# Kernel tuning notes

Hardware: AMD Instinct MI355X
Metric: run time of the kernel (lower is better)

The kernel has to match this reference:

```python
import jax, jax.numpy as jnp
import numpy as np

KSIZE = 3
STRIDE = 1
NEG_INF = -jnp.inf


def semiconv_maxmin(x, kernel, stride=STRIDE):
    """Tropical (max-min) 2D convolution, 'same' padding with -inf.

    out[n,o,i,j] = max over (c,kh,kw) of min(x_pad[n,c,i*s+kh,j*s+kw], kernel[o,c,kh,kw])
    """
    N, C, H, W = x.shape
    O, _, K, _ = kernel.shape
    p = K - 1
    top = p // 2
    bottom = p - top
    xp = jnp.pad(x, ((0, 0), (0, 0), (top, bottom), (top, bottom)),
                 constant_values=NEG_INF)
    Ho = (H + p - K) // stride + 1
    Wo = (W + p - K) // stride + 1
    out = jnp.full((N, O, Ho, Wo), NEG_INF, dtype=x.dtype)
    # Unrolled loop over the K*K taps (small, fixed); vectorized over n,o,c,h,w.
    for kh in range(K):
        for kw in range(K):
            xs = xp[:, :, kh:kh + stride * Ho:stride, kw:kw + stride * Wo:stride]  # [N,C,Ho,Wo]
            w = kernel[:, :, kh, kw]                                # [O,C]
            cand = jnp.minimum(xs[:, None], w[None, :, :, None, None])  # [N,O,C,Ho,Wo]
            out = jnp.maximum(out, jnp.max(cand, axis=2))
    return out


def setup_inputs() -> dict:
    key = jax.random.key(0)
    k1, k2 = jax.random.split(key)
    x = jax.random.normal(k1, (8, 32, 112, 112), dtype=jnp.float32)
    kernel = jax.random.normal(k2, (32, 32, KSIZE, KSIZE), dtype=jnp.float32)
    return {"x": x, "kernel": kernel}


def reference(x, kernel):
    return semiconv_maxmin(x, kernel, STRIDE)
```

## Files before the change

### kernel.cpp

```cpp
#include <hip/hip_runtime.h>
#include <math.h>

#define C_IN  32
#define O_OUT 32
#define HIMG  112
#define WIMG  112
#define HW    (HIMG * WIMG)
#define TS    8
#define NCP   16
#define XROW  12
#define XPLANE (10 * XROW)
#define WSLOT 12
#define WSTRIDE 196
#define OBLK  16
#define NW    (O_OUT * NCP * WSLOT)

typedef _Float16 h2 __attribute__((ext_vector_type(2)));

static __device__ __forceinline__ h2 h2min(h2 a, h2 b) {
    h2 r; asm("v_pk_min_f16 %0, %1, %2" : "=v"(r) : "v"(a), "v"(b)); return r;
}
static __device__ __forceinline__ h2 h2max(h2 a, h2 b) {
    h2 r; asm("v_pk_max_f16 %0, %1, %2" : "=v"(r) : "v"(a), "v"(b)); return r;
}

static __device__ __forceinline__ h2 asH2(float f) {
    union { float f; h2 h; } u; u.f = f; return u.h;
}
static __device__ __forceinline__ float asF(h2 h) {
    union { h2 h; float f; } u; u.h = h; return u.f;
}

__global__ void prep_weights(const float* __restrict__ kern, h2* __restrict__ wp)
{
    int idx = blockIdx.x * 256 + threadIdx.x;
    if (idx >= NW) return;
    int k  = idx % WSLOT;
    int cp = (idx / WSLOT) & (NCP - 1);
    int o  = idx / (WSLOT * NCP);
    float a = -INFINITY, b = -INFINITY;
    if (k < 9) {
        a = kern[(o * C_IN + 2 * cp    ) * 9 + k];
        b = kern[(o * C_IN + 2 * cp + 1) * 9 + k];
    }
    h2 v; v.x = (_Float16)a; v.y = (_Float16)b;
    wp[idx] = v;
}

struct Tile {
    h2 xr[4][10];
    h2 w[9];
};

static __device__ __forceinline__ void load_tile(Tile& t, const h2* __restrict__ xp,
                                                 const h2* __restrict__ wq)
{
    #pragma unroll
    for (int q = 0; q < 4; ++q) {
        const h2* rp = xp + q * XROW;
        float4 a = *(const float4*)rp;
        float4 b = *(const float4*)(rp + 4);
        float2 c = *(const float2*)(rp + 8);
        t.xr[q][0] = asH2(a.x); t.xr[q][1] = asH2(a.y);
        t.xr[q][2] = asH2(a.z); t.xr[q][3] = asH2(a.w);
        t.xr[q][4] = asH2(b.x); t.xr[q][5] = asH2(b.y);
        t.xr[q][6] = asH2(b.z); t.xr[q][7] = asH2(b.w);
        t.xr[q][8] = asH2(c.x); t.xr[q][9] = asH2(c.y);
    }
    float4 wa = *(const float4*)wq;
    float4 wb = *(const float4*)(wq + 4);
    float  wc = *(const float*)(wq + 8);
    t.w[0] = asH2(wa.x); t.w[1] = asH2(wa.y); t.w[2] = asH2(wa.z); t.w[3] = asH2(wa.w);
    t.w[4] = asH2(wb.x); t.w[5] = asH2(wb.y); t.w[6] = asH2(wb.z); t.w[7] = asH2(wb.w);
    t.w[8] = asH2(wc);
}

static __device__ __forceinline__ void compute_tile(const Tile& t, h2 acc[2][8])
{
    #pragma unroll
    for (int rr = 0; rr < 2; ++rr) {
        #pragma unroll
        for (int j = 0; j < 8; ++j) {
            h2 t0 = h2min(t.xr[rr    ][j    ], t.w[0]);
            h2 t1 = h2min(t.xr[rr    ][j + 1], t.w[1]);
            h2 t2 = h2min(t.xr[rr    ][j + 2], t.w[2]);
            h2 t3 = h2min(t.xr[rr + 1][j    ], t.w[3]);
            h2 t4 = h2min(t.xr[rr + 1][j + 1], t.w[4]);
            h2 t5 = h2min(t.xr[rr + 1][j + 2], t.w[5]);
            h2 t6 = h2min(t.xr[rr + 2][j    ], t.w[6]);
            h2 t7 = h2min(t.xr[rr + 2][j + 1], t.w[7]);
            h2 t8 = h2min(t.xr[rr + 2][j + 2], t.w[8]);
            h2 r0 = h2max(h2max(t0, t1), t2);
            h2 r1 = h2max(h2max(t3, t4), t5);
            h2 r2 = h2max(h2max(t6, t7), t8);
            acc[rr][j] = h2max(acc[rr][j], h2max(h2max(r0, r1), r2));
        }
    }
}

__global__ __launch_bounds__(256, 4) void semiconv_kernel(
    const float* __restrict__ x, const h2* __restrict__ wp,
    float* __restrict__ out)
{
    __shared__ h2 xs[NCP * XPLANE];
    __shared__ h2 ws[OBLK * WSTRIDE];

    const int tid = threadIdx.x;
    const int tj0 = blockIdx.x * TS;
    const int ti0 = blockIdx.y * TS;
    const int n   = blockIdx.z >> 1;
    const int o0  = (blockIdx.z & 1) * OBLK;
    const float* xn = x + (size_t)n * (C_IN * HW);

    #pragma unroll
    for (int i = 0; i < 3; ++i) {
        int chunk = i * 256 + tid;
        int oL    = chunk / 48;
        int rem   = chunk - oL * 48;
        float4 v  = *(const float4*)&wp[(size_t)((o0 + oL) * 48 + rem) * 4];
        *(float4*)&ws[oL * WSTRIDE + rem * 4] = v;
    }
    #pragma unroll 1
    for (int idx = tid; idx < NCP * XPLANE; idx += 256) {
        int cp  = idx / XPLANE;
        int rem = idx - cp * XPLANE;
        int r   = rem / XROW;
        int col = rem - r * XROW;
        int gi = ti0 - 1 + r, gj = tj0 - 1 + col;
        float a = -INFINITY, b = -INFINITY;
        if (col < 10 && (unsigned)gi < (unsigned)HIMG && (unsigned)gj < (unsigned)WIMG) {
            const float* p = xn + (size_t)(2 * cp) * HW + gi * WIMG + gj;
            a = p[0];
            b = p[HW];
        }
        h2 v; v.x = (_Float16)a; v.y = (_Float16)b;
        xs[idx] = v;
    }
    __syncthreads();

    const int lane = tid & 63;
    const int wv   = tid >> 6;
    const int oL   = lane & 15;
    const int prg  = lane >> 4;
    const int o    = o0 + oL;

    h2 ninf2; ninf2.x = (_Float16)(-INFINITY); ninf2.y = (_Float16)(-INFINITY);
    h2 acc[2][8];
    #pragma unroll
    for (int rr = 0; rr < 2; ++rr)
        #pragma unroll
        for (int j = 0; j < 8; ++j) acc[rr][j] = ninf2;

    const h2* xpl = &xs[(wv * 4) * XPLANE + (2 * prg) * XROW];
    const h2* wql = &ws[oL * WSTRIDE + (wv * 4) * WSLOT];

    Tile t0, t1, t2, t3;
    load_tile(t0, xpl + 0 * XPLANE, wql + 0 * WSLOT);
    load_tile(t1, xpl + 1 * XPLANE, wql + 1 * WSLOT);
    compute_tile(t0, acc);
    load_tile(t2, xpl + 2 * XPLANE, wql + 2 * WSLOT);
    compute_tile(t1, acc);
    load_tile(t3, xpl + 3 * XPLANE, wql + 3 * WSLOT);
    compute_tile(t2, acc);
    compute_tile(t3, acc);

    __syncthreads();
    if (wv != 0) {
        h2* dst = &ws[(wv - 1) * 1024 + lane * 16];
        float4 p0, p1, p2, p3;
        p0.x = asF(acc[0][0]); p0.y = asF(acc[0][1]); p0.z = asF(acc[0][2]); p0.w = asF(acc[0][3]);
        p1.x = asF(acc[0][4]); p1.y = asF(acc[0][5]); p1.z = asF(acc[0][6]); p1.w = asF(acc[0][7]);
        p2.x = asF(acc[1][0]); p2.y = asF(acc[1][1]); p2.z = asF(acc[1][2]); p2.w = asF(acc[1][3]);
        p3.x = asF(acc[1][4]); p3.y = asF(acc[1][5]); p3.z = asF(acc[1][6]); p3.w = asF(acc[1][7]);
        ((float4*)dst)[0] = p0; ((float4*)dst)[1] = p1;
        ((float4*)dst)[2] = p2; ((float4*)dst)[3] = p3;
    }
    __syncthreads();
    if (wv == 0) {
        #pragma unroll
        for (int r = 0; r < 3; ++r) {
            const h2* src = &ws[r * 1024 + lane * 16];
            #pragma unroll
            for (int half = 0; half < 2; ++half) {
                float4 pa = ((const float4*)src)[half * 2];
                float4 pb = ((const float4*)src)[half * 2 + 1];
                acc[half][0] = h2max(acc[half][0], asH2(pa.x));
                acc[half][1] = h2max(acc[half][1], asH2(pa.y));
                acc[half][2] = h2max(acc[half][2], asH2(pa.z));
                acc[half][3] = h2max(acc[half][3], asH2(pa.w));
                acc[half][4] = h2max(acc[half][4], asH2(pb.x));
                acc[half][5] = h2max(acc[half][5], asH2(pb.y));
                acc[half][6] = h2max(acc[half][6], asH2(pb.z));
                acc[half][7] = h2max(acc[half][7], asH2(pb.w));
            }
        }
        float* op = out + (((size_t)n * O_OUT + o) * HIMG + (ti0 + 2 * prg)) * WIMG + tj0;
        #pragma unroll
        for (int rr = 0; rr < 2; ++rr) {
            float4 v0, v1;
            v0.x = (float)(acc[rr][0].x > acc[rr][0].y ? acc[rr][0].x : acc[rr][0].y);
            v0.y = (float)(acc[rr][1].x > acc[rr][1].y ? acc[rr][1].x : acc[rr][1].y);
            v0.z = (float)(acc[rr][2].x > acc[rr][2].y ? acc[rr][2].x : acc[rr][2].y);
            v0.w = (float)(acc[rr][3].x > acc[rr][3].y ? acc[rr][3].x : acc[rr][3].y);
            v1.x = (float)(acc[rr][4].x > acc[rr][4].y ? acc[rr][4].x : acc[rr][4].y);
            v1.y = (float)(acc[rr][5].x > acc[rr][5].y ? acc[rr][5].x : acc[rr][5].y);
            v1.z = (float)(acc[rr][6].x > acc[rr][6].y ? acc[rr][6].x : acc[rr][6].y);
            v1.w = (float)(acc[rr][7].x > acc[rr][7].y ? acc[rr][7].x : acc[rr][7].y);
            *(float4*)(op + rr * WIMG)     = v0;
            *(float4*)(op + rr * WIMG + 4) = v1;
        }
    }
}

extern "C" void kernel_launch(void* const* d_in, const int* in_sizes, int n_in,
                              void* d_out, int out_size, void* d_ws, size_t ws_size,
                              hipStream_t stream) {
    const float* x    = (const float*)d_in[0];
    const float* kern = (const float*)d_in[1];
    float* out        = (float*)d_out;
    h2* wp            = (h2*)d_ws;

    prep_weights<<<dim3((NW + 255) / 256), dim3(256), 0, stream>>>(kern, wp);
    dim3 grid(WIMG / TS, HIMG / TS, 8 * 2);
    semiconv_kernel<<<grid, dim3(256), 0, stream>>>(x, wp, out);
}
```

Baseline: 54.73 us.

## Pre-pack input into halo-padded fp16 tiles in a separate kernel

Adds a pack_x kernel that converts x into per-tile, halo-padded, channel-paired fp16 blocks in workspace, so the main kernel copies its 16x10x12 tile with two coalesced float4 loads per thread. This replaces the scattered per-element fp32 gathers, bounds checks and conversions, which were repeated for each of the two output-channel halves. The cost is an extra kernel launch and an extra pass that writes and rereads about 1.7x the halo-expanded input. It falls back to the old path when the workspace is too small.

```diff
diff --git a/kernel.cpp b/kernel.cpp
--- a/kernel.cpp
+++ b/kernel.cpp
@@ -7,9 +7,12 @@
 #define WIMG  112
 #define HW    (HIMG * WIMG)
 #define TS    8
+#define NT    14
 #define NCP   16
 #define XROW  12
 #define XPLANE (10 * XROW)
+#define XTILE (NCP * XPLANE)
+#define NXT   (8 * NT * NT * XTILE)
 #define WSLOT 12
 #define WSTRIDE 196
 #define OBLK  16
@@ -45,6 +48,28 @@
     }
     h2 v; v.x = (_Float16)a; v.y = (_Float16)b;
     wp[idx] = v;
+}
+
+__global__ void pack_x(const float* __restrict__ x, h2* __restrict__ xt)
+{
+    int idx = blockIdx.x * 256 + threadIdx.x;
+    if (idx >= NXT) return;
+    int col = idx % XROW;
+    int r   = (idx / XROW) % 10;
+    int cp  = (idx / XPLANE) & (NCP - 1);
+    int tj  = (idx / XTILE) % NT;
+    int ti  = (idx / (XTILE * NT)) % NT;
+    int n   = idx / (XTILE * NT * NT);
+    int gi  = ti * TS + r - 1;
+    int gj  = tj * TS + col - 1;
+    float a = -INFINITY, b = -INFINITY;
+    if (col < 10 && (unsigned)gi < (unsigned)HIMG && (unsigned)gj < (unsigned)WIMG) {
+        const float* p = x + ((size_t)(n * C_IN + 2 * cp) * HIMG + gi) * WIMG + gj;
+        a = p[0];
+        b = p[HW];
+    }
+    h2 v; v.x = (_Float16)a; v.y = (_Float16)b;
+    xt[idx] = v;
 }
 
 struct Tile {
@@ -98,9 +123,10 @@
     }
 }
 
-__global__ __launch_bounds__(256, 4) void semiconv_kernel(
-    const float* __restrict__ x, const h2* __restrict__ wp,
-    float* __restrict__ out)
+template<bool TILED>
+__global__ __launch_bounds__(256, 4) void semiconv_tpl(
+    const float* __restrict__ x, const h2* __restrict__ xt,
+    const h2* __restrict__ wp, float* __restrict__ out)
 {
     __shared__ h2 xs[NCP * XPLANE];
     __shared__ h2 ws[OBLK * WSTRIDE];
@@ -110,7 +136,6 @@
     const int ti0 = blockIdx.y * TS;
     const int n   = blockIdx.z >> 1;
     const int o0  = (blockIdx.z & 1) * OBLK;
-    const float* xn = x + (size_t)n * (C_IN * HW);
 
     #pragma unroll
     for (int i = 0; i < 3; ++i) {
@@ -120,21 +145,30 @@
         float4 v  = *(const float4*)&wp[(size_t)((o0 + oL) * 48 + rem) * 4];
         *(float4*)&ws[oL * WSTRIDE + rem * 4] = v;
     }
-    #pragma unroll 1
-    for (int idx = tid; idx < NCP * XPLANE; idx += 256) {
-        int cp  = idx / XPLANE;
-        int rem = idx - cp * XPLANE;
-        int r   = rem / XROW;
-        int col = rem - r * XROW;
-        int gi = ti0 - 1 + r, gj = tj0 - 1 + col;
-        float a = -INFINITY, b = -INFINITY;
-        if (col < 10 && (unsigned)gi < (unsigned)HIMG && (unsigned)gj < (unsigned)WIMG) {
-            const float* p = xn + (size_t)(2 * cp) * HW + gi * WIMG + gj;
-            a = p[0];
-            b = p[HW];
-        }
-        h2 v; v.x = (_Float16)a; v.y = (_Float16)b;
-        xs[idx] = v;
+    if constexpr (TILED) {
+        const float4* xtp = (const float4*)(xt
+            + (size_t)((n * NT + blockIdx.y) * NT + blockIdx.x) * XTILE);
+        float4* xsp = (float4*)xs;
+        xsp[tid] = xtp[tid];
+        if (tid < 480 - 256) xsp[256 + tid] = xtp[256 + tid];
+    } else {
+        const float* xn = x + (size_t)n * (C_IN * HW);
+        #pragma unroll 1
+        for (int idx = tid; idx < NCP * XPLANE; idx += 256) {
+            int cp  = idx / XPLANE;
+            int rem = idx - cp * XPLANE;
+            int r   = rem / XROW;
+            int col = rem - r * XROW;
+            int gi = ti0 - 1 + r, gj = tj0 - 1 + col;
+            float a = -INFINITY, b = -INFINITY;
+            if (col < 10 && (unsigned)gi < (unsigned)HIMG && (unsigned)gj < (unsigned)WIMG) {
+                const float* p = xn + (size_t)(2 * cp) * HW + gi * WIMG + gj;
+                a = p[0];
+                b = p[HW];
+            }
+            h2 v; v.x = (_Float16)a; v.y = (_Float16)b;
+            xs[idx] = v;
+        }
     }
     __syncthreads();
 
@@ -219,8 +253,17 @@
     const float* kern = (const float*)d_in[1];
     float* out        = (float*)d_out;
     h2* wp            = (h2*)d_ws;
+    h2* xt            = (h2*)((char*)d_ws + NW * 4);
+
+    const size_t need = (size_t)NW * 4 + (size_t)NXT * 4;
+    const bool tiled = ws_size >= need;
 
     prep_weights<<<dim3((NW + 255) / 256), dim3(256), 0, stream>>>(kern, wp);
-    dim3 grid(WIMG / TS, HIMG / TS, 8 * 2);
-    semiconv_kernel<<<grid, dim3(256), 0, stream>>>(x, wp, out);
-}
+    dim3 grid(NT, NT, 8 * 2);
+    if (tiled) {
+        pack_x<<<dim3((NXT + 255) / 256), dim3(256), 0, stream>>>(x, xt);
+        semiconv_tpl<true ><<<grid, dim3(256), 0, stream>>>(x, xt, wp, out);
+    } else {
+        semiconv_tpl<false><<<grid, dim3(256), 0, stream>>>(x, xt, wp, out);
+    }
+}
```

Result: no change. 54.56 us (-0.3%).
